# Performance work log

Measured on AMD Instinct MI355X. Metric: run time of the kernel, lower is better.

## Reference

```python
import jax, jax.numpy as jnp
import numpy as np

K_NB = 16
HID = 64
CIN = 128
EPS = 1e-5


def knn_idx(q, t, k):
    # q [B,N,3] queries, t [B,M,3] targets -> idx [B,N,k] into targets
    d = (jnp.sum(q * q, -1)[:, :, None] + jnp.sum(t * t, -1)[:, None, :]
         - 2.0 * jnp.einsum('bnd,bmd->bnm', q, t))
    _, idx = jax.lax.top_k(-d, k)
    return idx


def gather(feat, idx):
    # feat [B,C,M], idx [B,N,K] -> [B,C,N,K]
    return jax.vmap(lambda f, i: f[:, i])(feat, idx)


def conv1x1(x, W, b):
    # x [B,C,N,K], W [O,C], b [O]
    return jnp.einsum('oc,bcnk->bonk', W, x) + b[None, :, None, None]


def group_norm(x, gamma, beta, groups):
    B, C, N, K = x.shape
    xg = x.reshape(B, groups, C // groups, N, K)
    m = xg.mean(axis=(2, 3, 4), keepdims=True)
    v = xg.var(axis=(2, 3, 4), keepdims=True)
    xg = (xg - m) / jnp.sqrt(v + EPS)
    x = xg.reshape(B, C, N, K)
    return x * gamma[None, :, None, None] + beta[None, :, None, None]


def leaky(x):
    return jnp.where(x >= 0, x, 0.1 * x)


def setup_inputs() -> dict:
    key = jax.random.key(0)
    ks = jax.random.split(key, 20)
    B, N = 2, 4096
    d = {
        'xyz0': jax.random.normal(ks[0], (B, 3, N), jnp.float32),
        'xyz1': jax.random.normal(ks[1], (B, 3, N), jnp.float32),
        'state': jax.random.normal(ks[2], (B, HID, N), jnp.float32),
        'corr0': jax.random.normal(ks[3], (B, HID, N), jnp.float32),
        'feat0': jax.random.normal(ks[4], (B, CIN, N), jnp.float32),
        'feat1': jax.random.normal(ks[5], (B, CIN, N), jnp.float32),
        'flow0': jax.random.normal(ks[6], (B, 3, N), jnp.float32),
        # flow_layer: SetConv(3, [64,64]) -> convs take 3+3=6 then 64 in-chans
        'fw1': jax.random.normal(ks[7], (64, 6), jnp.float32) * 0.05,
        'fb1': jnp.zeros((64,), jnp.float32),
        'fg1': jnp.ones((64,), jnp.float32),
        'fbe1': jnp.zeros((64,), jnp.float32),
        'fw2': jax.random.normal(ks[8], (64, 64), jnp.float32) * 0.05,
        'fb2': jnp.zeros((64,), jnp.float32),
        'fg2': jnp.ones((64,), jnp.float32),
        'fbe2': jnp.zeros((64,), jnp.float32),
        # GRU gates: SetConv in_feat = hid(64)+(hid+64=128)=192, +3 = 195 -> 64, no act
        'wz': jax.random.normal(ks[9], (HID, 195), jnp.float32) * 0.05,
        'bz': jnp.zeros((HID,), jnp.float32),
        'wr': jax.random.normal(ks[10], (HID, 195), jnp.float32) * 0.05,
        'br': jnp.zeros((HID,), jnp.float32),
        'wq': jax.random.normal(ks[11], (HID, 195), jnp.float32) * 0.05,
        'bq': jnp.zeros((HID,), jnp.float32),
        # interp weight_net: 2*128+3=259 -> 128 -> 64
        'wa1': jax.random.normal(ks[12], (CIN, 2 * CIN + 3), jnp.float32) * 0.05,
        'ba1': jnp.zeros((CIN,), jnp.float32),
        'wa2': jax.random.normal(ks[13], (HID, CIN), jnp.float32) * 0.05,
        'ba2': jnp.zeros((HID,), jnp.float32),
    }
    return d


def reference(xyz0, xyz1, state, corr0, feat0, feat1, flow0,
              fw1, fb1, fg1, fbe1, fw2, fb2, fg2, fbe2,
              wz, bz, wr, br, wq, bq, wa1, ba1, wa2, ba2):
    xyz0_t = xyz0.transpose(0, 2, 1)  # [B,N,3]
    xyz1_t = xyz1.transpose(0, 2, 1)

    # ---- flow_layer: SetConv (KNN, N==npoint so new_xyz = xyz0) ----
    idx0 = knn_idx(xyz0_t, xyz0_t, K_NB)              # [B,N,K]
    gxyz0 = gather(xyz0, idx0) - xyz0[:, :, :, None]  # [B,3,N,K]
    h = jnp.concatenate([gather(flow0, idx0), gxyz0], axis=1)  # [B,6,N,K]
    h = leaky(group_norm(conv1x1(h, fw1, fb1), fg1, fbe1, 64 // 16))
    h = leaky(group_norm(conv1x1(h, fw2, fb2), fg2, fbe2, 64 // 16))
    flow_feat = h.max(axis=3)  # [B,64,N]

    # ---- iter_layer: SetGRU over xyz0 neighbors ----
    feat_g = jnp.concatenate([corr0, flow_feat], axis=1)  # [B,128,N]

    def gate(f, W, b):
        g = jnp.concatenate([gather(f, idx0), gxyz0], axis=1)
        return conv1x1(g, W, b).max(axis=3)  # [B,64,N]

    hid_in = jnp.concatenate([feat_g, state], axis=1)  # [B,192,N]
    z = jax.nn.sigmoid(gate(hid_in, wz, bz))
    r = jax.nn.sigmoid(gate(hid_in, wr, br))
    q = jnp.tanh(gate(jnp.concatenate([feat_g, r * state], axis=1), wq, bq))
    next_state = (1.0 - z) * state + z * q  # [B,64,N]

    # ---- align_layer: SetInterp (queries xyz1, targets xyz0) ----
    idx1 = knn_idx(xyz1_t, xyz0_t, K_NB)
    gv = gather(next_state, idx1)                        # [B,64,N,K]
    gx = gather(xyz0, idx1) - xyz1[:, :, :, None]        # [B,3,N,K]
    gf = jnp.concatenate([
        gather(feat0, idx1),
        jnp.broadcast_to(feat1[:, :, :, None], feat1.shape + (K_NB,))], axis=1)
    w = conv1x1(jnp.concatenate([gf, gx], axis=1), wa1, ba1)
    w = conv1x1(leaky(w), wa2, ba2)
    w = jax.nn.softmax(w, axis=3)
    return jnp.sum(gv * w, axis=3)  # [B,64,N]
```

## Files before the change

kernel.cpp:

```cpp
#include <hip/hip_runtime.h>

#define B_SZ 2
#define CAP 320

__device__ __forceinline__ int rfl(int x) { return __builtin_amdgcn_readfirstlane(x); }
__device__ __forceinline__ float leaky(float v) { return v >= 0.f ? v : 0.1f * v; }

__launch_bounds__(256)
__global__ void pack_kernel(const float* __restrict__ xyz, float4* __restrict__ out, int N)
{
  int b = blockIdx.y;
  int i = blockIdx.x * 256 + threadIdx.x;
  if (i >= N) return;
  const float* p = xyz + (size_t)b * 3 * N;
  float x = p[i], y = p[N + i], z = p[2 * N + i];
  out[(size_t)b * N + i] = make_float4(x, y, z, x * x + y * y + z * z);
}

__launch_bounds__(256)
__global__ void knn_thresh_kernel(const float4* __restrict__ pk,
    const float* __restrict__ q0, const float* __restrict__ q1,
    float* __restrict__ t0arr, int N, int PN)
{
  __shared__ float bounds[4][64];
  const int lane = threadIdx.x & 63;
  const int wav = rfl(threadIdx.x >> 6);
  const int qg = blockIdx.x * 64 + lane;
  const bool src1 = qg >= PN;
  const int qloc = src1 ? qg - PN : qg;
  const int b = qloc / N;
  const int n = qloc - b * N;
  const float* qb = (src1 ? q1 : q0) + (size_t)b * 3 * N;
  const float qx = qb[n], qy = qb[N + n], qz = qb[2 * N + n];
  const float qq = qx * qx + qy * qy + qz * qz;
  const int SEG = N >> 4;
  const float4* pb = pk + (size_t)b * N + (size_t)wav * (N >> 2);

  float m0 = 3.0e38f, m1 = 3.0e38f, m2 = 3.0e38f, m3 = 3.0e38f;
  for (int i = 0; i < SEG; ++i) {
    float4 v0 = pb[i];
    float4 v1 = pb[SEG + i];
    float4 v2 = pb[2 * SEG + i];
    float4 v3 = pb[3 * SEG + i];
    m0 = fminf(m0, (qq + v0.w) - 2.0f * (qx * v0.x + qy * v0.y + qz * v0.z));
    m1 = fminf(m1, (qq + v1.w) - 2.0f * (qx * v1.x + qy * v1.y + qz * v1.z));
    m2 = fminf(m2, (qq + v2.w) - 2.0f * (qx * v2.x + qy * v2.y + qz * v2.z));
    m3 = fminf(m3, (qq + v3.w) - 2.0f * (qx * v3.x + qy * v3.y + qz * v3.z));
  }
  bounds[wav][lane] = fmaxf(fmaxf(m0, m1), fmaxf(m2, m3));
  __syncthreads();
  if (wav == 0) {
    float t0 = fmaxf(fmaxf(bounds[0][lane], bounds[1][lane]),
                     fmaxf(bounds[2][lane], bounds[3][lane]));
    t0arr[qg] = t0;
  }
}

__launch_bounds__(256)
__global__ void knn_select_kernel(const float4* __restrict__ pk,
    const float* __restrict__ q0, const float* __restrict__ q1,
    const float* __restrict__ t0arr,
    int* __restrict__ idx0, int* __restrict__ idx1, int N, int PN)
{
  __shared__ __align__(16) float4 ts[1024];
  __shared__ uint2 buf[4][CAP];
  const int lane = threadIdx.x & 63, wav = rfl(threadIdx.x >> 6);
  const int qg = blockIdx.x * 4 + wav;
  const bool src1 = qg >= PN;
  const int qloc = src1 ? qg - PN : qg;
  const int b = qloc / N;
  const int n = qloc - b * N;
  const float* qb = (src1 ? q1 : q0) + (size_t)b * 3 * N;
  const float qx = qb[n], qy = qb[N + n], qz = qb[2 * N + n];
  const float qq = qx * qx + qy * qy + qz * qz;
  float t0 = t0arr[qg];
  t0 += fabsf(t0) * 1e-4f + 1e-12f;
  const float4* pb = pk + (size_t)b * N;

  int cnt = 0;
  for (int ch = 0; ch < N; ch += 1024) {
    __syncthreads();
    for (int i = threadIdx.x; i < 1024; i += 256) ts[i] = pb[ch + i];
    __syncthreads();
    for (int sub = 0; sub < 16; ++sub) {
      float4 v = ts[sub * 64 + lane];
      float key = (qq + v.w) - 2.0f * (qx * v.x + qy * v.y + qz * v.z);
      bool qf = key <= t0;
      unsigned long long mask = __ballot(qf);
      if (mask) {
        unsigned lo = __builtin_amdgcn_mbcnt_lo((unsigned)mask, 0u);
        unsigned pre = __builtin_amdgcn_mbcnt_hi((unsigned)(mask >> 32), lo);
        if (qf) {
          unsigned slot = (unsigned)cnt + pre;
          if (slot < (unsigned)CAP)
            buf[wav][slot] = make_uint2(__float_as_uint(key),
                                        (unsigned)(ch + sub * 64 + lane));
        }
        cnt += (int)__popcll(mask);
      }
    }
  }
  int C = cnt < CAP ? cnt : CAP;
  int* op = src1 ? idx1 : idx0;
  size_t base = ((size_t)b * N + n) * 16;

  if (C <= 64) {
    float kd = 3.0e38f; int ki = 0x7fffffff;
    if (lane < C) { uint2 u = buf[wav][lane]; kd = __uint_as_float(u.x); ki = (int)u.y; }
    int rank = 0;
    for (int j = 0; j < C; ++j) {
      uint2 u = buf[wav][j];
      float kj = __uint_as_float(u.x); int ij = (int)u.y;
      rank += ((kj < kd) || (kj == kd && ij < ki)) ? 1 : 0;
    }
    if (lane < C && rank < 16) op[base + rank] = ki;
  } else {
    float kd[5]; int ki[5]; int rank[5] = {0, 0, 0, 0, 0};
#pragma unroll
    for (int e = 0; e < 5; ++e) {
      int j = e * 64 + lane;
      if (j < C) { uint2 u = buf[wav][j]; kd[e] = __uint_as_float(u.x); ki[e] = (int)u.y; }
      else { kd[e] = 3.0e38f; ki[e] = 0x7fffffff; }
    }
    for (int j = 0; j < C; ++j) {
      uint2 u = buf[wav][j];
      float kj = __uint_as_float(u.x); int ij = (int)u.y;
#pragma unroll
      for (int e = 0; e < 5; ++e)
        rank[e] += ((kj < kd[e]) || (kj == kd[e] && ij < ki[e])) ? 1 : 0;
    }
#pragma unroll
    for (int e = 0; e < 5; ++e)
      if (e * 64 + lane < C && rank[e] < 16) op[base + rank[e]] = ki[e];
  }
}

__launch_bounds__(256)
__global__ void prep_w_kernel(const float* __restrict__ wz, const float* __restrict__ wr,
    const float* __restrict__ wq, const float* __restrict__ wa1, const float* __restrict__ wa2,
    const float* __restrict__ bz, const float* __restrict__ br,
    float* __restrict__ WtZR, float* __restrict__ WtQ,
    float* __restrict__ WtU, float* __restrict__ WtV, float* __restrict__ WtA2,
    float* __restrict__ bZR)
{
  int job = blockIdx.x;
  int tid = threadIdx.x;
  if (job == 0) {
    for (int e = tid; e < 195 * 128; e += 256) {
      int k = e >> 7, o = e & 127;
      const float* w = (o < 64) ? wz : wr;
      WtZR[(size_t)k * 128 + o] = w[(size_t)(o & 63) * 195 + k];
    }
    if (tid < 128) bZR[tid] = (tid < 64) ? bz[tid] : br[tid - 64];
  } else if (job == 1) {
    for (int e = tid; e < 195 * 64; e += 256) {
      int k = e >> 6, o = e & 63;
      WtQ[(size_t)k * 64 + o] = wq[(size_t)o * 195 + k];
    }
  } else if (job == 2) {
    for (int e = tid; e < 131 * 128; e += 256) {
      int k = e >> 7, o = e & 127;
      int col = (k < 128) ? k : 256 + (k - 128);
      WtU[(size_t)k * 128 + o] = wa1[(size_t)o * 259 + col];
    }
  } else if (job == 3) {
    for (int e = tid; e < 131 * 128; e += 256) {
      int k = e >> 7, o = e & 127;
      float v = (k < 128) ? wa1[(size_t)o * 259 + 128 + k]
                          : -wa1[(size_t)o * 259 + 256 + (k - 128)];
      WtV[(size_t)k * 128 + o] = v;
    }
  } else {
    for (int e = tid; e < 128 * 64; e += 256) {
      int c = e >> 6, o = e & 63;
      WtA2[e] = wa2[(size_t)o * 128 + c];
    }
  }
}

#define KC 66
__launch_bounds__(256)
__global__ void projT_kernel(const float* __restrict__ Wt, int K, int WOUT,
    const float* __restrict__ bias, float* __restrict__ out,
    int N, int PN,
    const float* __restrict__ s0, int c0, int l0,
    const float* __restrict__ s1, int c1, int l1,
    const float* __restrict__ s2, int c2, int l2,
    const float* __restrict__ s3, int c3, int l3)
{
  __shared__ __align__(16) float Ws[KC][68];
  __shared__ __align__(16) float Xs[KC][68];
  const int n0 = blockIdx.x * 64;
  const int oo = blockIdx.y * 64;
  const int b = n0 / N;
  const int nn0 = n0 - b * N;
  const int tid = threadIdx.x;
  const int tx = tid & 15, ty = tid >> 4;
  const int o4 = tx * 4, n4 = ty * 4;
  float acc[4][4];
#pragma unroll
  for (int i = 0; i < 4; ++i)
#pragma unroll
    for (int j = 0; j < 4; ++j)
      acc[i][j] = bias ? bias[oo + o4 + j] : 0.0f;

  const int e01 = c0 + c1, e012 = c0 + c1 + c2;
  for (int k0 = 0; k0 < K; k0 += KC) {
    const int kc = min(KC, K - k0);
    __syncthreads();
    for (int e = tid; e < kc * 64; e += 256) {
      int k = e >> 6, o = e & 63;
      Ws[k][o] = Wt[(size_t)(k0 + k) * WOUT + oo + o];
    }
    for (int e = tid; e < kc * 64; e += 256) {
      int k = e >> 6, j = e & 63;
      int c = k0 + k;
      float v;
      if (c < c0)        v = l0 ? s0[(size_t)c * PN + n0 + j]
                                : s0[((size_t)b * c0 + c) * N + nn0 + j];
      else if (c < e01)  { int cc = c - c0;
                           v = l1 ? s1[(size_t)cc * PN + n0 + j]
                                  : s1[((size_t)b * c1 + cc) * N + nn0 + j]; }
      else if (c < e012) { int cc = c - e01;
                           v = l2 ? s2[(size_t)cc * PN + n0 + j]
                                  : s2[((size_t)b * c2 + cc) * N + nn0 + j]; }
      else               { int cc = c - e012;
                           v = l3 ? s3[(size_t)cc * PN + n0 + j]
                                  : s3[((size_t)b * c3 + cc) * N + nn0 + j]; }
      Xs[k][j] = v;
    }
    __syncthreads();
#pragma unroll 2
    for (int k = 0; k < kc; ++k) {
      float4 wv = *(const float4*)&Ws[k][o4];
      float4 xv = *(const float4*)&Xs[k][n4];
      acc[0][0] = fmaf(xv.x, wv.x, acc[0][0]); acc[0][1] = fmaf(xv.x, wv.y, acc[0][1]);
      acc[0][2] = fmaf(xv.x, wv.z, acc[0][2]); acc[0][3] = fmaf(xv.x, wv.w, acc[0][3]);
      acc[1][0] = fmaf(xv.y, wv.x, acc[1][0]); acc[1][1] = fmaf(xv.y, wv.y, acc[1][1]);
      acc[1][2] = fmaf(xv.y, wv.z, acc[1][2]); acc[1][3] = fmaf(xv.y, wv.w, acc[1][3]);
      acc[2][0] = fmaf(xv.z, wv.x, acc[2][0]); acc[2][1] = fmaf(xv.z, wv.y, acc[2][1]);
      acc[2][2] = fmaf(xv.z, wv.z, acc[2][2]); acc[2][3] = fmaf(xv.z, wv.w, acc[2][3]);
      acc[3][0] = fmaf(xv.w, wv.x, acc[3][0]); acc[3][1] = fmaf(xv.w, wv.y, acc[3][1]);
      acc[3][2] = fmaf(xv.w, wv.z, acc[3][2]); acc[3][3] = fmaf(xv.w, wv.w, acc[3][3]);
    }
  }
#pragma unroll
  for (int i = 0; i < 4; ++i) {
    float4 r = make_float4(acc[i][0], acc[i][1], acc[i][2], acc[i][3]);
    *(float4*)&out[(size_t)(n0 + n4 + i) * WOUT + oo + o4] = r;
  }
}

__launch_bounds__(256)
__global__ void projUV_kernel(const float* __restrict__ WtU, const float* __restrict__ WtV,
    const float* __restrict__ ba1, float* __restrict__ Uo, float* __restrict__ Vo,
    int N, int PN,
    const float* __restrict__ feat0, const float* __restrict__ feat1,
    const float* __restrict__ x0, const float* __restrict__ x1)
{
  __shared__ __align__(16) float Ws[KC][68];
  __shared__ __align__(16) float Xs[KC][68];
  const int z = blockIdx.z;
  const float* Wt = z ? WtV : WtU;
  const float* bias = z ? ba1 : 0;
  float* out = z ? Vo : Uo;
  const float* s0 = z ? feat1 : feat0;
  const float* s1 = z ? x1 : x0;
  const int K = 131, WOUT = 128, c0 = 128;
  const int n0 = blockIdx.x * 64;
  const int oo = blockIdx.y * 64;
  const int b = n0 / N;
  const int nn0 = n0 - b * N;
  const int tid = threadIdx.x;
  const int tx = tid & 15, ty = tid >> 4;
  const int o4 = tx * 4, n4 = ty * 4;
  float acc[4][4];
#pragma unroll
  for (int i = 0; i < 4; ++i)
#pragma unroll
    for (int j = 0; j < 4; ++j)
      acc[i][j] = bias ? bias[oo + o4 + j] : 0.0f;

  for (int k0 = 0; k0 < K; k0 += KC) {
    const int kc = min(KC, K - k0);
    __syncthreads();
    for (int e = tid; e < kc * 64; e += 256) {
      int k = e >> 6, o = e & 63;
      Ws[k][o] = Wt[(size_t)(k0 + k) * WOUT + oo + o];
    }
    for (int e = tid; e < kc * 64; e += 256) {
      int k = e >> 6, j = e & 63;
      int c = k0 + k;
      float v;
      if (c < c0) v = s0[((size_t)b * c0 + c) * N + nn0 + j];
      else        v = s1[((size_t)b * 3 + (c - c0)) * N + nn0 + j];
      Xs[k][j] = v;
    }
    __syncthreads();
#pragma unroll 2
    for (int k = 0; k < kc; ++k) {
      float4 wv = *(const float4*)&Ws[k][o4];
      float4 xv = *(const float4*)&Xs[k][n4];
      acc[0][0] = fmaf(xv.x, wv.x, acc[0][0]); acc[0][1] = fmaf(xv.x, wv.y, acc[0][1]);
      acc[0][2] = fmaf(xv.x, wv.z, acc[0][2]); acc[0][3] = fmaf(xv.x, wv.w, acc[0][3]);
      acc[1][0] = fmaf(xv.y, wv.x, acc[1][0]); acc[1][1] = fmaf(xv.y, wv.y, acc[1][1]);
      acc[1][2] = fmaf(xv.y, wv.z, acc[1][2]); acc[1][3] = fmaf(xv.y, wv.w, acc[1][3]);
      acc[2][0] = fmaf(xv.z, wv.x, acc[2][0]); acc[2][1] = fmaf(xv.z, wv.y, acc[2][1]);
      acc[2][2] = fmaf(xv.z, wv.z, acc[2][2]); acc[2][3] = fmaf(xv.z, wv.w, acc[2][3]);
      acc[3][0] = fmaf(xv.w, wv.x, acc[3][0]); acc[3][1] = fmaf(xv.w, wv.y, acc[3][1]);
      acc[3][2] = fmaf(xv.w, wv.z, acc[3][2]); acc[3][3] = fmaf(xv.w, wv.w, acc[3][3]);
    }
  }
#pragma unroll
  for (int i = 0; i < 4; ++i) {
    float4 r = make_float4(acc[i][0], acc[i][1], acc[i][2], acc[i][3]);
    *(float4*)&out[(size_t)(n0 + n4 + i) * WOUT + oo + o4] = r;
  }
}

__device__ __forceinline__ void seg_accumL(const float* __restrict__ p, int cnt,
    const float* __restrict__ WL, int sC, int sN, long n0, float acc[4])
{
#pragma unroll 4
  for (int c = 0; c < cnt; ++c) {
    float w = WL[c];
    const float* pp = p + (size_t)c * sC + (size_t)n0 * sN;
#pragma unroll
    for (int m = 0; m < 4; ++m)
      acc[m] = fmaf(w, pp[(size_t)m * sN], acc[m]);
  }
}

template<int WP>
__launch_bounds__(256)
__global__ void proj_kernel(
    const float* __restrict__ W0, const float* __restrict__ bias,
    float* __restrict__ out, int OUTS, int wld, int N,
    const float* __restrict__ s0, int c0, int w0,
    const float* __restrict__ s1, int c1, int w1)
{
  __shared__ float Wl[64 * WP];
  const int b = blockIdx.y;
  const int lane = threadIdx.x & 63;
  const int wav = rfl(threadIdx.x >> 6);
  for (int r = wav; r < 64; r += 4)
    for (int c = lane; c < c0; c += 64)
      Wl[r * WP + c] = W0[(size_t)r * wld + w0 + c];
  for (int r = wav; r < 64; r += 4)
    for (int c = lane; c < c1; c += 64)
      Wl[r * WP + c0 + c] = W0[(size_t)r * wld + w1 + c];
  __syncthreads();
  const long n0 = ((long)blockIdx.x * 4 + wav) * 4;
  float bv = bias ? bias[lane] : 0.0f;
  float acc[4] = {bv, bv, bv, bv};
  const float* WL = &Wl[lane * WP];
  seg_accumL(s0 + (size_t)b * c0 * N, c0, WL, N, 1, n0, acc);
  seg_accumL(s1 + (size_t)b * c1 * N, c1, WL + c0, N, 1, n0, acc);
#pragma unroll
  for (int m = 0; m < 4; ++m)
    out[((size_t)b * N + n0 + m) * OUTS + lane] = acc[m];
}

__launch_bounds__(256)
__global__ void gn1_stats_kernel(const float* __restrict__ G1, const float* __restrict__ xyz0,
    const float* __restrict__ fw1, const int* __restrict__ idx0,
    float* __restrict__ stats1, int N)
{
  __shared__ float red[4][4][2];
  int b = blockIdx.y;
  int lane = threadIdx.x & 63, wav = rfl(threadIdx.x >> 6);
  float wg0 = fw1[lane * 6 + 3], wg1 = fw1[lane * 6 + 4], wg2 = fw1[lane * 6 + 5];
  const float* xb = xyz0 + (size_t)b * 3 * N;
  float sum = 0.f, sq = 0.f;
  for (int n = blockIdx.x * 4 + wav; n < N; n += gridDim.x * 4) {
    const int* ip = idx0 + ((size_t)b * N + n) * 16;
    float bx = wg0 * xb[n] + wg1 * xb[N + n] + wg2 * xb[2 * N + n];
#pragma unroll
    for (int k = 0; k < 16; ++k) {
      int m = ip[k];
      float y = G1[((size_t)b * N + m) * 64 + lane] - bx;
      sum += y; sq += y * y;
    }
  }
#pragma unroll
  for (int off = 1; off < 16; off <<= 1) {
    sum += __shfl_xor(sum, off, 64);
    sq += __shfl_xor(sq, off, 64);
  }
  int g = lane >> 4;
  if ((lane & 15) == 0) { red[wav][g][0] = sum; red[wav][g][1] = sq; }
  __syncthreads();
  if (threadIdx.x < 8) {
    int gg = threadIdx.x >> 1, s = threadIdx.x & 1;
    float v = red[0][gg][s] + red[1][gg][s] + red[2][gg][s] + red[3][gg][s];
    atomicAdd(&stats1[(b * 4 + gg) * 2 + s], v);
  }
}

__launch_bounds__(256, 2)
__global__ void conv2_kernel(const float* __restrict__ G1, const float* __restrict__ xyz0,
    const float* __restrict__ fw1, const int* __restrict__ idx0,
    const float* __restrict__ fw2, const float* __restrict__ fb2,
    const float* __restrict__ fg1, const float* __restrict__ fbe1,
    const float* __restrict__ raw1, float cnt,
    float* __restrict__ y2max, float* __restrict__ y2min,
    float* __restrict__ stats2, int N)
{
  __shared__ __align__(16) float x2[4][16][64];
  __shared__ float red[4][4][2];
  const int b = blockIdx.y;
  const int lane = threadIdx.x & 63;
  const int wav = rfl(threadIdx.x >> 6);
  float4 w[16];
#pragma unroll
  for (int i = 0; i < 16; ++i) w[i] = *(const float4*)&fw2[lane * 64 + i * 4];
  float wg0 = fw1[lane * 6 + 3], wg1 = fw1[lane * 6 + 4], wg2 = fw1[lane * 6 + 5];
  const int g = lane >> 4;
  float s_ = raw1[(b * 4 + g) * 2], q_ = raw1[(b * 4 + g) * 2 + 1];
  float mu1 = s_ / cnt;
  float inv1 = rsqrtf(q_ / cnt - mu1 * mu1 + 1e-5f);
  float sc1 = fg1[lane] * inv1;
  float sh1 = fbe1[lane] - mu1 * sc1;
  float fb2l = fb2[lane];
  const float* xb = xyz0 + (size_t)b * 3 * N;
  float sum = 0.f, sq = 0.f;
  for (int n = blockIdx.x * 4 + wav; n < N; n += gridDim.x * 4) {
    const int* ip = idx0 + ((size_t)b * N + n) * 16;
    float bx = wg0 * xb[n] + wg1 * xb[N + n] + wg2 * xb[2 * N + n];
#pragma unroll
    for (int k = 0; k < 16; ++k) {
      int m = ip[k];
      float y = G1[((size_t)b * N + m) * 64 + lane] - bx;
      x2[wav][k][lane] = leaky(y * sc1 + sh1);
    }
    float acc[16];
#pragma unroll
    for (int k = 0; k < 16; ++k) acc[k] = fb2l;
#pragma unroll
    for (int c4 = 0; c4 < 16; ++c4) {
      float4 w4 = w[c4];
#pragma unroll
      for (int k = 0; k < 16; ++k) {
        float4 x4 = *(const float4*)&x2[wav][k][c4 * 4];
        acc[k] = fmaf(w4.x, x4.x, acc[k]);
        acc[k] = fmaf(w4.y, x4.y, acc[k]);
        acc[k] = fmaf(w4.z, x4.z, acc[k]);
        acc[k] = fmaf(w4.w, x4.w, acc[k]);
      }
    }
    float mx = -3.0e38f, mn = 3.0e38f;
#pragma unroll
    for (int k = 0; k < 16; ++k) {
      mx = fmaxf(mx, acc[k]); mn = fminf(mn, acc[k]);
      sum += acc[k]; sq += acc[k] * acc[k];
    }
    y2max[((size_t)b * N + n) * 64 + lane] = mx;
    y2min[((size_t)b * N + n) * 64 + lane] = mn;
  }
#pragma unroll
  for (int off = 1; off < 16; off <<= 1) {
    sum += __shfl_xor(sum, off, 64);
    sq += __shfl_xor(sq, off, 64);
  }
  if ((lane & 15) == 0) { red[wav][g][0] = sum; red[wav][g][1] = sq; }
  __syncthreads();
  if (threadIdx.x < 8) {
    int gg = threadIdx.x >> 1, s = threadIdx.x & 1;
    float v = red[0][gg][s] + red[1][gg][s] + red[2][gg][s] + red[3][gg][s];
    atomicAdd(&stats2[(b * 4 + gg) * 2 + s], v);
  }
}

__launch_bounds__(256)
__global__ void flow_feat_kernel(const float* __restrict__ y2max, const float* __restrict__ y2min,
    const float* __restrict__ raw2, float cnt,
    const float* __restrict__ fg2, const float* __restrict__ fbe2,
    float* __restrict__ ff_t, int N, int PN)
{
  size_t i = (size_t)blockIdx.x * blockDim.x + threadIdx.x;
  if (i >= (size_t)B_SZ * N * 64) return;
  int c = i & 63;
  size_t pn = i >> 6;
  int b = (int)(pn / N);
  int g = c >> 4;
  float s_ = raw2[(b * 4 + g) * 2], q_ = raw2[(b * 4 + g) * 2 + 1];
  float mu = s_ / cnt;
  float inv = rsqrtf(q_ / cnt - mu * mu + 1e-5f);
  float sc = fg2[c] * inv;
  float sh = fbe2[c] - mu * sc;
  float y = (sc >= 0.0f) ? y2max[i] : y2min[i];
  ff_t[(size_t)c * PN + pn] = leaky(y * sc + sh);
}

__launch_bounds__(256)
__global__ void gate_zr_kernel(const float* __restrict__ Szr,
    const float* __restrict__ wz, const float* __restrict__ wr,
    const float* __restrict__ xyz0, const float* __restrict__ state,
    const int* __restrict__ idx0,
    float* __restrict__ zo, float* __restrict__ rs_t, int N, int PN)
{
  int b = blockIdx.y;
  int lane = threadIdx.x & 63, wav = rfl(threadIdx.x >> 6);
  float wz0 = wz[lane * 195 + 192], wz1 = wz[lane * 195 + 193], wz2 = wz[lane * 195 + 194];
  float wr0 = wr[lane * 195 + 192], wr1 = wr[lane * 195 + 193], wr2 = wr[lane * 195 + 194];
  const float* xb = xyz0 + (size_t)b * 3 * N;
  for (int n = blockIdx.x * 4 + wav; n < N; n += gridDim.x * 4) {
    const int* ip = idx0 + ((size_t)b * N + n) * 16;
    float u0 = xb[n], u1 = xb[N + n], u2 = xb[2 * N + n];
    float xz = wz0 * u0 + wz1 * u1 + wz2 * u2;
    float xr = wr0 * u0 + wr1 * u1 + wr2 * u2;
    float mz = -3.0e38f, mr = -3.0e38f;
#pragma unroll
    for (int k = 0; k < 16; ++k) {
      size_t mo = ((size_t)b * N + ip[k]) * 128 + lane;
      mz = fmaxf(mz, Szr[mo]);
      mr = fmaxf(mr, Szr[mo + 64]);
    }
    size_t no = ((size_t)b * N + n) * 64 + lane;
    float z = 1.f / (1.f + expf(-(mz - xz)));
    float r = 1.f / (1.f + expf(-(mr - xr)));
    zo[no] = z;
    rs_t[(size_t)lane * PN + (size_t)b * N + n] = r * state[((size_t)b * 64 + lane) * N + n];
  }
}

__launch_bounds__(256)
__global__ void gate_q_ns_kernel(const float* __restrict__ Sq, const float* __restrict__ wq,
    const float* __restrict__ xyz0, const float* __restrict__ zo,
    const float* __restrict__ state, const int* __restrict__ idx0,
    float* __restrict__ ns, int N)
{
  int b = blockIdx.y;
  int lane = threadIdx.x & 63, wav = rfl(threadIdx.x >> 6);
  float wq0 = wq[lane * 195 + 192], wq1 = wq[lane * 195 + 193], wq2 = wq[lane * 195 + 194];
  const float* xb = xyz0 + (size_t)b * 3 * N;
  for (int n = blockIdx.x * 4 + wav; n < N; n += gridDim.x * 4) {
    const int* ip = idx0 + ((size_t)b * N + n) * 16;
    float xq = wq0 * xb[n] + wq1 * xb[N + n] + wq2 * xb[2 * N + n];
    float mq = -3.0e38f;
#pragma unroll
    for (int k = 0; k < 16; ++k)
      mq = fmaxf(mq, Sq[((size_t)b * N + ip[k]) * 64 + lane]);
    size_t no = ((size_t)b * N + n) * 64 + lane;
    float q = tanhf(mq - xq);
    float z = zo[no];
    float st = state[((size_t)b * 64 + lane) * N + n];
    ns[no] = (1.f - z) * st + z * q;
  }
}

__launch_bounds__(256, 2)
__global__ void align_kernel(const float* __restrict__ U, const float* __restrict__ V,
    const float* __restrict__ WtA2, const float* __restrict__ ba2,
    const float* __restrict__ ns, const int* __restrict__ idx1,
    float* __restrict__ out, int N)
{
  __shared__ __align__(16) float Xs[64][128];
  __shared__ __align__(16) float Ws[128][64];
  const int b = blockIdx.y;
  const int tid = threadIdx.x;
  const int lane = tid & 63;
  const int wav = rfl(tid >> 6);

  for (int e = tid; e < 2048; e += 256) {
    int c = e >> 4, o4 = (e & 15) << 2;
    *(float4*)&Ws[c][o4] = *(const float4*)&WtA2[(c << 6) + o4];
  }

  const int n = blockIdx.x * 4 + wav;
  int mkreg = 0;
  {
    const int* ip = idx1 + ((size_t)b * N + n) * 16;
    if (lane < 16) mkreg = ip[lane];
  }
  const int c4l = lane & 31;
  const int half = lane >> 5;
  float4 v4 = *(const float4*)&V[(((size_t)b * N + n) << 7) + (c4l << 2)];
  for (int k0 = 0; k0 < 16; k0 += 2) {
    int k = k0 + half;
    int m = __shfl(mkreg, k);
    float4 u4 = *(const float4*)&U[(((size_t)b * N + m) << 7) + (c4l << 2)];
    float4 xv;
    xv.x = leaky(u4.x + v4.x);
    xv.y = leaky(u4.y + v4.y);
    xv.z = leaky(u4.z + v4.z);
    xv.w = leaky(u4.w + v4.w);
    int row = (wav << 4) + k;
    *(float4*)&Xs[row][(c4l ^ (row & 7)) << 2] = xv;
  }
  __syncthreads();

  const int tx = tid & 15, ty = tid >> 4;
  const int o4 = tx << 2, r0 = ty << 2;
  float4 bav = *(const float4*)&ba2[o4];
  float acc[4][4];
#pragma unroll
  for (int i = 0; i < 4; ++i) {
    acc[i][0] = bav.x; acc[i][1] = bav.y; acc[i][2] = bav.z; acc[i][3] = bav.w;
  }
  for (int c4 = 0; c4 < 32; ++c4) {
    float4 wv0 = *(const float4*)&Ws[c4 * 4 + 0][o4];
    float4 wv1 = *(const float4*)&Ws[c4 * 4 + 1][o4];
    float4 wv2 = *(const float4*)&Ws[c4 * 4 + 2][o4];
    float4 wv3 = *(const float4*)&Ws[c4 * 4 + 3][o4];
#pragma unroll
    for (int i = 0; i < 4; ++i) {
      int row = r0 + i;
      float4 xv = *(const float4*)&Xs[row][(c4 ^ (row & 7)) << 2];
      acc[i][0] = fmaf(xv.x, wv0.x, acc[i][0]);
      acc[i][1] = fmaf(xv.x, wv0.y, acc[i][1]);
      acc[i][2] = fmaf(xv.x, wv0.z, acc[i][2]);
      acc[i][3] = fmaf(xv.x, wv0.w, acc[i][3]);
      acc[i][0] = fmaf(xv.y, wv1.x, acc[i][0]);
      acc[i][1] = fmaf(xv.y, wv1.y, acc[i][1]);
      acc[i][2] = fmaf(xv.y, wv1.z, acc[i][2]);
      acc[i][3] = fmaf(xv.y, wv1.w, acc[i][3]);
      acc[i][0] = fmaf(xv.z, wv2.x, acc[i][0]);
      acc[i][1] = fmaf(xv.z, wv2.y, acc[i][1]);
      acc[i][2] = fmaf(xv.z, wv2.z, acc[i][2]);
      acc[i][3] = fmaf(xv.z, wv2.w, acc[i][3]);
      acc[i][0] = fmaf(xv.w, wv3.x, acc[i][0]);
      acc[i][1] = fmaf(xv.w, wv3.y, acc[i][1]);
      acc[i][2] = fmaf(xv.w, wv3.z, acc[i][2]);
      acc[i][3] = fmaf(xv.w, wv3.w, acc[i][3]);
    }
  }

  float m_[4];
#pragma unroll
  for (int j = 0; j < 4; ++j) {
    float m = fmaxf(fmaxf(acc[0][j], acc[1][j]), fmaxf(acc[2][j], acc[3][j]));
    m = fmaxf(m, __shfl_xor(m, 16, 64));
    m = fmaxf(m, __shfl_xor(m, 32, 64));
    m_[j] = m;
  }
  float e_[4][4], s_[4];
#pragma unroll
  for (int j = 0; j < 4; ++j) {
    float s = 0.f;
#pragma unroll
    for (int i = 0; i < 4; ++i) { e_[i][j] = expf(acc[i][j] - m_[j]); s += e_[i][j]; }
    s += __shfl_xor(s, 16, 64);
    s += __shfl_xor(s, 32, 64);
    s_[j] = s;
  }
  float o_[4] = {0.f, 0.f, 0.f, 0.f};
#pragma unroll
  for (int i = 0; i < 4; ++i) {
    int k = (r0 + i) & 15;
    int m = __shfl(mkreg, k);
    float4 nsv = *(const float4*)&ns[(((size_t)b * N + m) << 6) + o4];
    o_[0] = fmaf(e_[i][0], nsv.x, o_[0]);
    o_[1] = fmaf(e_[i][1], nsv.y, o_[1]);
    o_[2] = fmaf(e_[i][2], nsv.z, o_[2]);
    o_[3] = fmaf(e_[i][3], nsv.w, o_[3]);
  }
#pragma unroll
  for (int j = 0; j < 4; ++j) {
    o_[j] += __shfl_xor(o_[j], 16, 64);
    o_[j] += __shfl_xor(o_[j], 32, 64);
  }
  if ((lane >> 4) == 0) {
#pragma unroll
    for (int j = 0; j < 4; ++j)
      out[((size_t)b * 64 + o4 + j) * N + n] = o_[j] / s_[j];
  }
}

extern "C" void kernel_launch(void* const* d_in, const int* in_sizes, int n_in,
                              void* d_out, int out_size, void* d_ws, size_t ws_size,
                              hipStream_t stream) {
  (void)n_in; (void)out_size; (void)ws_size;
  const float* xyz0 = (const float*)d_in[0];
  const float* xyz1 = (const float*)d_in[1];
  const float* state = (const float*)d_in[2];
  const float* corr0 = (const float*)d_in[3];
  const float* feat0 = (const float*)d_in[4];
  const float* feat1 = (const float*)d_in[5];
  const float* flow0 = (const float*)d_in[6];
  const float* fw1 = (const float*)d_in[7];
  const float* fb1 = (const float*)d_in[8];
  const float* fg1 = (const float*)d_in[9];
  const float* fbe1 = (const float*)d_in[10];
  const float* fw2 = (const float*)d_in[11];
  const float* fb2 = (const float*)d_in[12];
  const float* fg2 = (const float*)d_in[13];
  const float* fbe2 = (const float*)d_in[14];
  const float* wz = (const float*)d_in[15];
  const float* bz = (const float*)d_in[16];
  const float* wr = (const float*)d_in[17];
  const float* br = (const float*)d_in[18];
  const float* wq = (const float*)d_in[19];
  const float* bq = (const float*)d_in[20];
  const float* wa1 = (const float*)d_in[21];
  const float* ba1 = (const float*)d_in[22];
  const float* wa2 = (const float*)d_in[23];
  const float* ba2 = (const float*)d_in[24];
  float* out = (float*)d_out;

  const int N = in_sizes[0] / (3 * B_SZ);
  const int PN = B_SZ * N;
  char* wsb = (char*)d_ws;
  size_t off = 0;
  auto take = [&](size_t bytes) -> char* {
    char* p = wsb + off;
    off += (bytes + 255) & ~(size_t)255;
    return p;
  };
  float* U    = (float*)take((size_t)PN * 128 * 4);
  float* V    = (float*)take((size_t)PN * 128 * 4);
  float* Szr  = (float*)take((size_t)PN * 128 * 4);
  float4* pk0 = (float4*)take((size_t)PN * 4 * 4);
  int*   idx0 = (int*)  take((size_t)PN * 16 * 4);
  int*   idx1 = (int*)  take((size_t)PN * 16 * 4);
  float* t0a  = (float*)take((size_t)2 * PN * 4);
  float* G1   = (float*)take((size_t)PN * 64 * 4);
  float* y2mx = (float*)take((size_t)PN * 64 * 4);
  float* y2mn = (float*)take((size_t)PN * 64 * 4);
  float* ff_t = (float*)take((size_t)PN * 64 * 4);
  float* Sq   = (float*)take((size_t)PN * 64 * 4);
  float* zg   = (float*)take((size_t)PN * 64 * 4);
  float* rs_t = (float*)take((size_t)PN * 64 * 4);
  float* ns   = (float*)take((size_t)PN * 64 * 4);
  float* WtZR = (float*)take(195 * 128 * 4);
  float* WtQ  = (float*)take(195 * 64 * 4);
  float* WtU  = (float*)take(131 * 128 * 4);
  float* WtV  = (float*)take(131 * 128 * 4);
  float* WtA2 = (float*)take(128 * 64 * 4);
  float* bZR  = (float*)take(128 * 4);
  float* stats = (float*)take(256);
  float* raw1 = stats, *raw2 = stats + 16;

  const float cntv = 16.0f * N * 16.0f;

  hipMemsetAsync(raw1, 0, 32 * sizeof(float), stream);

  pack_kernel<<<dim3((N + 255) / 256, B_SZ), 256, 0, stream>>>(xyz0, pk0, N);
  prep_w_kernel<<<5, 256, 0, stream>>>(wz, wr, wq, wa1, wa2, bz, br,
      WtZR, WtQ, WtU, WtV, WtA2, bZR);
  knn_thresh_kernel<<<dim3(2 * PN / 64), 256, 0, stream>>>(pk0, xyz0, xyz1, t0a, N, PN);
  knn_select_kernel<<<dim3(2 * PN / 4), 256, 0, stream>>>(pk0, xyz0, xyz1, t0a,
      idx0, idx1, N, PN);

  proj_kernel<7><<<dim3(N / 16, B_SZ), 256, 0, stream>>>(
      fw1, fb1, G1, 64, 6, N, flow0, 3, 0, xyz0, 3, 3);

  gn1_stats_kernel<<<dim3(256, B_SZ), 256, 0, stream>>>(G1, xyz0, fw1, idx0, raw1, N);
  conv2_kernel<<<dim3(512, B_SZ), 256, 0, stream>>>(G1, xyz0, fw1, idx0, fw2, fb2, fg1, fbe1,
      raw1, cntv, y2mx, y2mn, raw2, N);
  flow_feat_kernel<<<dim3((unsigned)((size_t)PN * 64 / 256)), 256, 0, stream>>>(
      y2mx, y2mn, raw2, cntv, fg2, fbe2, ff_t, N, PN);

  projT_kernel<<<dim3(PN / 64, 2), 256, 0, stream>>>(WtZR, 195, 128, bZR, Szr, N, PN,
      corr0, 64, 0,  ff_t, 64, 1,  state, 64, 0,  xyz0, 3, 0);

  gate_zr_kernel<<<dim3(256, B_SZ), 256, 0, stream>>>(Szr, wz, wr, xyz0, state, idx0, zg, rs_t, N, PN);

  projT_kernel<<<dim3(PN / 64, 1), 256, 0, stream>>>(WtQ, 195, 64, bq, Sq, N, PN,
      corr0, 64, 0,  ff_t, 64, 1,  rs_t, 64, 1,  xyz0, 3, 0);

  gate_q_ns_kernel<<<dim3(256, B_SZ), 256, 0, stream>>>(Sq, wq, xyz0, zg, state, idx0, ns, N);

  projUV_kernel<<<dim3(PN / 64, 2, 2), 256, 0, stream>>>(WtU, WtV, ba1, U, V, N, PN,
      feat0, feat1, xyz0, xyz1);

  align_kernel<<<dim3(N / 4, B_SZ), 256, 0, stream>>>(U, V, WtA2, ba2, ns, idx1, out, N);
}
```

Baseline: 376.6 us.

## Split KNN threshold across 16 segment-threads per query; drop LDS staging in select

The threshold kernel now gives each query 16 threads, each scanning one segment, instead of one lane scanning four segments. A block covers 16 queries instead of 64, and the 16 segment minima are max-reduced through shared memory. This raises parallelism and launches four times as many blocks. The select kernel drops the shared-memory tile and its __syncthreads, so each wave reads packed points straight from global/L2. That removes block-wide barriers but gives up reuse of the tile across the block's four waves.

```diff
diff --git a/kernel.cpp b/kernel.cpp
--- a/kernel.cpp
+++ b/kernel.cpp
@@ -22,10 +22,11 @@
     const float* __restrict__ q0, const float* __restrict__ q1,
     float* __restrict__ t0arr, int N, int PN)
 {
-  __shared__ float bounds[4][64];
-  const int lane = threadIdx.x & 63;
-  const int wav = rfl(threadIdx.x >> 6);
-  const int qg = blockIdx.x * 64 + lane;
+  __shared__ float sm[16][16];
+  const int tid = threadIdx.x;
+  const int q = tid & 15;
+  const int s = tid >> 4;
+  const int qg = blockIdx.x * 16 + q;
   const bool src1 = qg >= PN;
   const int qloc = src1 ? qg - PN : qg;
   const int b = qloc / N;
@@ -34,25 +35,21 @@
   const float qx = qb[n], qy = qb[N + n], qz = qb[2 * N + n];
   const float qq = qx * qx + qy * qy + qz * qz;
   const int SEG = N >> 4;
-  const float4* pb = pk + (size_t)b * N + (size_t)wav * (N >> 2);
-
-  float m0 = 3.0e38f, m1 = 3.0e38f, m2 = 3.0e38f, m3 = 3.0e38f;
+  const float4* ps = pk + (size_t)b * N + (size_t)s * SEG;
+
+  float m = 3.0e38f;
+#pragma unroll 4
   for (int i = 0; i < SEG; ++i) {
-    float4 v0 = pb[i];
-    float4 v1 = pb[SEG + i];
-    float4 v2 = pb[2 * SEG + i];
-    float4 v3 = pb[3 * SEG + i];
-    m0 = fminf(m0, (qq + v0.w) - 2.0f * (qx * v0.x + qy * v0.y + qz * v0.z));
-    m1 = fminf(m1, (qq + v1.w) - 2.0f * (qx * v1.x + qy * v1.y + qz * v1.z));
-    m2 = fminf(m2, (qq + v2.w) - 2.0f * (qx * v2.x + qy * v2.y + qz * v2.z));
-    m3 = fminf(m3, (qq + v3.w) - 2.0f * (qx * v3.x + qy * v3.y + qz * v3.z));
-  }
-  bounds[wav][lane] = fmaxf(fmaxf(m0, m1), fmaxf(m2, m3));
+    float4 v = ps[i];
+    m = fminf(m, (qq + v.w) - 2.0f * (qx * v.x + qy * v.y + qz * v.z));
+  }
+  sm[s][q] = m;
   __syncthreads();
-  if (wav == 0) {
-    float t0 = fmaxf(fmaxf(bounds[0][lane], bounds[1][lane]),
-                     fmaxf(bounds[2][lane], bounds[3][lane]));
-    t0arr[qg] = t0;
+  if (tid < 16) {
+    float t0 = sm[0][tid];
+#pragma unroll
+    for (int ss = 1; ss < 16; ++ss) t0 = fmaxf(t0, sm[ss][tid]);
+    t0arr[blockIdx.x * 16 + tid] = t0;
   }
 }
 
@@ -62,7 +59,6 @@
     const float* __restrict__ t0arr,
     int* __restrict__ idx0, int* __restrict__ idx1, int N, int PN)
 {
-  __shared__ __align__(16) float4 ts[1024];
   __shared__ uint2 buf[4][CAP];
   const int lane = threadIdx.x & 63, wav = rfl(threadIdx.x >> 6);
   const int qg = blockIdx.x * 4 + wav;
@@ -78,26 +74,22 @@
   const float4* pb = pk + (size_t)b * N;
 
   int cnt = 0;
-  for (int ch = 0; ch < N; ch += 1024) {
-    __syncthreads();
-    for (int i = threadIdx.x; i < 1024; i += 256) ts[i] = pb[ch + i];
-    __syncthreads();
-    for (int sub = 0; sub < 16; ++sub) {
-      float4 v = ts[sub * 64 + lane];
-      float key = (qq + v.w) - 2.0f * (qx * v.x + qy * v.y + qz * v.z);
-      bool qf = key <= t0;
-      unsigned long long mask = __ballot(qf);
-      if (mask) {
-        unsigned lo = __builtin_amdgcn_mbcnt_lo((unsigned)mask, 0u);
-        unsigned pre = __builtin_amdgcn_mbcnt_hi((unsigned)(mask >> 32), lo);
-        if (qf) {
-          unsigned slot = (unsigned)cnt + pre;
-          if (slot < (unsigned)CAP)
-            buf[wav][slot] = make_uint2(__float_as_uint(key),
-                                        (unsigned)(ch + sub * 64 + lane));
-        }
-        cnt += (int)__popcll(mask);
+  const int NIT = N >> 6;
+  for (int it = 0; it < NIT; ++it) {
+    float4 v = pb[it * 64 + lane];
+    float key = (qq + v.w) - 2.0f * (qx * v.x + qy * v.y + qz * v.z);
+    bool qf = key <= t0;
+    unsigned long long mask = __ballot(qf);
+    if (mask) {
+      unsigned lo = __builtin_amdgcn_mbcnt_lo((unsigned)mask, 0u);
+      unsigned pre = __builtin_amdgcn_mbcnt_hi((unsigned)(mask >> 32), lo);
+      if (qf) {
+        unsigned slot = (unsigned)cnt + pre;
+        if (slot < (unsigned)CAP)
+          buf[wav][slot] = make_uint2(__float_as_uint(key),
+                                      (unsigned)(it * 64 + lane));
       }
+      cnt += (int)__popcll(mask);
     }
   }
   int C = cnt < CAP ? cnt : CAP;
@@ -738,7 +730,7 @@
   pack_kernel<<<dim3((N + 255) / 256, B_SZ), 256, 0, stream>>>(xyz0, pk0, N);
   prep_w_kernel<<<5, 256, 0, stream>>>(wz, wr, wq, wa1, wa2, bz, br,
       WtZR, WtQ, WtU, WtV, WtA2, bZR);
-  knn_thresh_kernel<<<dim3(2 * PN / 64), 256, 0, stream>>>(pk0, xyz0, xyz1, t0a, N, PN);
+  knn_thresh_kernel<<<dim3(2 * PN / 16), 256, 0, stream>>>(pk0, xyz0, xyz1, t0a, N, PN);
   knn_select_kernel<<<dim3(2 * PN / 4), 256, 0, stream>>>(pk0, xyz0, xyz1, t0a,
       idx0, idx1, N, PN);
 
```

Measured after the change: 366.6 us. -2.7%, faster.
